# Optimization experiments

Hardware: AMD Instinct MI355X
Metric: run time of the kernel (lower is better)

Reference implementation:

```python
import jax, jax.numpy as jnp
import numpy as np

B, S, H, L, C = 32, 512, 768, 512, 3  # batch, seq, hidden, max_length, num_classes


def _lin_init(k, fan_in, shape):
    return jax.random.normal(k, shape, jnp.float32) * (1.0 / np.sqrt(fan_in))


def setup_inputs() -> dict:
    key = jax.random.key(0)
    ks = jax.random.split(key, 18)
    return {
        "tokens": jax.random.normal(ks[0], (B, S, H), jnp.float32),
        # shared Q/K/V projections (used for both token- and feature-attention)
        "Wq": _lin_init(ks[1], H, (H, H)), "bq": jnp.zeros((H,), jnp.float32),
        "Wk": _lin_init(ks[2], H, (H, H)), "bk": jnp.zeros((H,), jnp.float32),
        "Wv": _lin_init(ks[3], H, (H, H)), "bv": jnp.zeros((H,), jnp.float32),
        # TSGSA: Linear(H,1)+ReLU gate over tokens
        "W_ts": _lin_init(ks[4], H, (H, 1)), "b_ts": jnp.zeros((1,), jnp.float32),
        # FSGSA: Linear(max_length,1)+ReLU gate over padded seq axis (also reused for FGSA per source bug)
        "W_fs": _lin_init(ks[5], L, (L, 1)), "b_fs": jnp.zeros((1,), jnp.float32),
        # TGSA: Linear(H,H)+Sigmoid gate
        "W_tg": _lin_init(ks[6], H, (H, H)), "b_tg": jnp.zeros((H,), jnp.float32),
        # fnn: Linear(7H,H) -> Linear(H,C)
        "W1": _lin_init(ks[7], 7 * H, (7 * H, H)), "b1": jnp.zeros((H,), jnp.float32),
        "W2": _lin_init(ks[8], H, (H, C)), "b2": jnp.zeros((C,), jnp.float32),
    }


def _ln(x):
    # LayerNorm over (seq, hidden) jointly, eps=1e-8; freshly-instantiated affine params are identity
    m = jnp.mean(x, axis=(1, 2), keepdims=True)
    v = jnp.var(x, axis=(1, 2), keepdims=True)
    return (x - m) * jax.lax.rsqrt(v + 1e-8)


def reference(tokens, Wq, bq, Wk, bk, Wv, bv, W_ts, b_ts, W_fs, b_fs, W_tg, b_tg, W1, b1, W2, b2):
    scale = 1.0 / np.sqrt(H)
    Q = tokens @ Wq + bq  # [B,S,H]
    K = tokens @ Wk + bk
    V = tokens @ Wv + bv
    # token-direction self-attention: softmax(Q K^T / sqrt(H)) V
    att = jax.nn.softmax(jnp.einsum('bsh,bth->bst', Q, K) * scale, axis=-1)  # [B,S,S]
    TSA = jnp.einsum('bst,bth->bsh', att, V)
    # feature-direction self-attention: V @ softmax(Q^T K / sqrt(H))
    attN = jax.nn.softmax(jnp.einsum('bsh,bsg->bhg', Q, K) * scale, axis=-1)  # [B,H,H]
    FSA = jnp.einsum('bsh,bhg->bsg', V, attN)
    # gate branches
    TSGSA = jax.nn.relu(tokens @ W_ts + b_ts) * tokens  # [B,S,1]*[B,S,H]
    tpad = jnp.pad(tokens.transpose(0, 2, 1), ((0, 0), (0, 0), (0, L - S)))  # [B,H,L]
    gate_f = jax.nn.relu(tpad @ W_fs + b_fs)  # [B,H,1]
    FSGSA = (gate_f * tokens.transpose(0, 2, 1)).transpose(0, 2, 1)  # [B,S,H]
    TGSA = jax.nn.sigmoid(tokens @ W_tg + b_tg) * tokens
    FGSA = FSGSA  # source bug: FGSA branch applies self.FSGSA, identical to FSGSA
    out_all = jnp.concatenate(
        [tokens, _ln(TSA), _ln(FSA), _ln(TGSA), _ln(FGSA), _ln(TSGSA), _ln(FSGSA)], axis=2)  # [B,S,7H]
    pooled = jnp.mean(out_all, axis=1)  # [B,7H]
    return (pooled @ W1 + b1) @ W2 + b2  # [B,C]
```

## Files before the change

kernel.cpp:

```cpp
#include <hip/hip_runtime.h>
#include <cmath>

typedef unsigned short u16;
typedef __attribute__((ext_vector_type(4))) float f32x4;
typedef __attribute__((ext_vector_type(4))) unsigned int u32x4;
typedef __attribute__((ext_vector_type(8))) __bf16 bf16x8;

__device__ __forceinline__ u16 f2b(float f) {
  unsigned int u = __builtin_bit_cast(unsigned int, f);
  return (u16)((u + 0x7fffu + ((u >> 16) & 1u)) >> 16);
}
__device__ __forceinline__ float b2f(u16 h) {
  unsigned int u = ((unsigned int)h) << 16;
  return __builtin_bit_cast(float, u);
}

__device__ __forceinline__ void glds16(const u16* g, u16* l) {
  __builtin_amdgcn_global_load_lds(
      (const __attribute__((address_space(1))) void*)g,
      (__attribute__((address_space(3))) void*)l, 16, 0, 0);
}

template <int EPI>
__global__ __launch_bounds__(256) void gemm_f_k(
    const u16* __restrict__ Ap, const u16* __restrict__ Bp, u16* __restrict__ Cp,
    u16* __restrict__ CpT, const float* __restrict__ bias,
    const u16* __restrict__ tokp, float* __restrict__ colsum,
    float* __restrict__ bstat, int K, int lda, int ldb, int ldc, long sA,
    long sB, long sC, float scale) {
  __shared__ alignas(16) u16 smem[4][4096];
  __shared__ float scol_s[128];
  __shared__ float sred[2];

  const int gx = gridDim.x, gxy = gx * gridDim.y;
  const int nwg = gxy * gridDim.z;
  int orig = (blockIdx.z * gridDim.y + blockIdx.y) * gx + blockIdx.x;
  int gwi = (orig & 7) * (nwg >> 3) + (orig >> 3);
  const int z = gwi / gxy;
  int rem = gwi - z * gxy;
  const int ty = rem / gx, tx = rem - ty * gx;
  const int tileM = ty << 7, tileN = tx << 7;

  const u16* Abase = Ap + (size_t)z * sA;
  const u16* Bbase = Bp + (size_t)z * sB;

  const int tid = threadIdx.x;
  const int lane = tid & 63, w = tid >> 6;
  const int wr = (w >> 1) << 6, wc = (w & 1) << 6;
  const int fr = lane & 15, fg = lane >> 4;

  f32x4 acc[4][4];
#pragma unroll
  for (int i = 0; i < 4; ++i)
#pragma unroll
    for (int j = 0; j < 4; ++j) acc[i][j] = (f32x4){0.f, 0.f, 0.f, 0.f};

  const int srow = (w << 5) + (lane >> 2);
  const int scol = (((lane & 3) ^ ((lane >> 3) & 3)) << 3);
  const u16* gA = Abase + (size_t)(tileM + srow) * lda + scol;
  const u16* gB = Bbase + (size_t)(tileN + srow) * ldb + scol;
  const int ldsw = (w << 5) * 32;

  auto STAGE = [&](int buf, int k0) {
    const u16* ga = gA + k0;
    const u16* gb = gB + k0;
    u16* la = &smem[buf * 2][ldsw];
    u16* lb = &smem[buf * 2 + 1][ldsw];
    glds16(ga, la);
    glds16(ga + (size_t)16 * lda, la + 512);
    glds16(gb, lb);
    glds16(gb + (size_t)16 * ldb, lb + 512);
  };

  const int col_off = ((fg ^ ((fr >> 1) & 3)) << 3);

  const int nt = K >> 5;
  STAGE(0, 0);
  int cur = 0;
  for (int t = 0; t < nt; ++t) {
    if (t + 1 < nt) {
      STAGE(cur ^ 1, (t + 1) << 5);
      asm volatile("s_waitcnt vmcnt(4)" ::: "memory");
    } else {
      asm volatile("s_waitcnt vmcnt(0)" ::: "memory");
    }
    __builtin_amdgcn_s_barrier();
    asm volatile("" ::: "memory");
    const u16* Ab = smem[cur * 2];
    const u16* Bb = smem[cur * 2 + 1];
    bf16x8 av[4], bw[4];
#pragma unroll
    for (int m = 0; m < 4; ++m)
      av[m] = *(const bf16x8*)&Ab[(wr + (m << 4) + fr) * 32 + col_off];
#pragma unroll
    for (int n = 0; n < 4; ++n)
      bw[n] = *(const bf16x8*)&Bb[(wc + (n << 4) + fr) * 32 + col_off];
#pragma unroll
    for (int m = 0; m < 4; ++m)
#pragma unroll
      for (int n = 0; n < 4; ++n)
        acc[m][n] =
            __builtin_amdgcn_mfma_f32_16x16x32_bf16(av[m], bw[n], acc[m][n], 0, 0, 0);
    asm volatile("" ::: "memory");
    __builtin_amdgcn_s_barrier();
    cur ^= 1;
  }

  if constexpr (EPI == 0) {
    const int cbuf = tileN / 768;
    const int nbase = tileN - cbuf * 768;
    u16* Cz = Cp + (size_t)cbuf * sC;
#pragma unroll
    for (int m = 0; m < 4; ++m) {
#pragma unroll
      for (int n = 0; n < 4; ++n) {
        const int gcol = tileN + wc + (n << 4) + fr;
        const int lcol = nbase + wc + (n << 4) + fr;
        const float bv2 = bias[gcol];
#pragma unroll
        for (int r = 0; r < 4; ++r) {
          const int grow = tileM + wr + (m << 4) + (fg << 2) + r;
          Cz[(size_t)grow * 768 + lcol] = f2b(acc[m][n][r] + bv2);
        }
      }
    }
    u16* tr = &smem[0][0];
    const int xr = fr << 3;
#pragma unroll
    for (int m = 0; m < 4; ++m) {
#pragma unroll
      for (int n = 0; n < 4; ++n) {
        const int gcol = tileN + wc + (n << 4) + fr;
        const float bv2 = bias[gcol];
        union { u16 u[4]; unsigned long long q; } pk;
#pragma unroll
        for (int r = 0; r < 4; ++r) pk.u[r] = f2b(acc[m][n][r] + bv2);
        const int rowb = wr + (m << 4) + (fg << 2);
        *(unsigned long long*)&tr[(wc + (n << 4) + fr) * 128 + (rowb ^ xr)] = pk.q;
      }
    }
    __syncthreads();
    u16* Ct = CpT + (size_t)cbuf * sC;
    const int col = tid >> 1, rh = (tid & 1) << 6;
    const int xc = (col & 15) << 3;
    const u16* trc = &tr[col * 128];
    u16* outc = &Ct[(size_t)(nbase + col) * 16384 + tileM];
#pragma unroll
    for (int i = 0; i < 8; ++i) {
      const int r0 = rh + (i << 3);
      *(u32x4*)&outc[r0] = *(const u32x4*)&trc[r0 ^ xc];
    }
  } else if constexpr (EPI == 1) {
    if (tid < 128) scol_s[tid] = 0.f;
    if (tid == 0) { sred[0] = 0.f; sred[1] = 0.f; }
    __syncthreads();
    float ls = 0.f, lq = 0.f;
#pragma unroll
    for (int n = 0; n < 4; ++n) {
      float cpart = 0.f;
      const int gcol = tileN + wc + (n << 4) + fr;
      const float bv2 = bias[gcol];
#pragma unroll
      for (int m = 0; m < 4; ++m) {
#pragma unroll
        for (int r = 0; r < 4; ++r) {
          const int grow = tileM + wr + (m << 4) + (fg << 2) + r;
          float g = 1.f / (1.f + __expf(-(acc[m][n][r] + bv2)));
          float v = g * b2f(tokp[(size_t)grow * 768 + gcol]);
          cpart += v; ls += v; lq += v * v;
        }
      }
      atomicAdd(&scol_s[wc + (n << 4) + fr], cpart);
    }
    atomicAdd(&sred[0], ls);
    atomicAdd(&sred[1], lq);
    __syncthreads();
    const int b = tileM >> 9;
    if (tid < 128) atomicAdd(&colsum[(size_t)b * 768 + tileN + tid], scol_s[tid]);
    if (tid == 0) {
      atomicAdd(&bstat[b], sred[0]);
      atomicAdd(&bstat[32 + b], sred[1]);
    }
  } else if constexpr (EPI == 2) {
    u16* Cz = Cp + (size_t)z * sC;
#pragma unroll
    for (int m = 0; m < 4; ++m) {
#pragma unroll
      for (int n = 0; n < 4; ++n) {
        const int gcol = tileN + wc + (n << 4) + fr;
#pragma unroll
        for (int r = 0; r < 4; ++r) {
          const int grow = tileM + wr + (m << 4) + (fg << 2) + r;
          Cz[(size_t)grow * ldc + gcol] = f2b(acc[m][n][r] * scale);
        }
      }
    }
  } else {
    if (tid < 128) scol_s[tid] = 0.f;
    if (tid == 0) { sred[0] = 0.f; sred[1] = 0.f; }
    __syncthreads();
    float ls = 0.f, lq = 0.f;
#pragma unroll
    for (int n = 0; n < 4; ++n) {
      float cpart = 0.f;
#pragma unroll
      for (int m = 0; m < 4; ++m) {
#pragma unroll
        for (int r = 0; r < 4; ++r) {
          float v = acc[m][n][r];
          cpart += v; ls += v; lq += v * v;
        }
      }
      atomicAdd(&scol_s[wc + (n << 4) + fr], cpart);
    }
    atomicAdd(&sred[0], ls);
    atomicAdd(&sred[1], lq);
    __syncthreads();
    if (tid < 128) atomicAdd(&colsum[(size_t)z * 768 + tileN + tid], scol_s[tid]);
    if (tid == 0) {
      atomicAdd(&bstat[z], sred[0]);
      atomicAdd(&bstat[32 + z], sred[1]);
    }
  }
}

__global__ __launch_bounds__(256) void cvt_row_k(
    const float* __restrict__ tok, u16* __restrict__ tokb,
    const float* __restrict__ Wts, const float* __restrict__ bts,
    float* __restrict__ gate_t, float* __restrict__ rowsum,
    float* __restrict__ rowsumsq) {
  const int w = threadIdx.x >> 6, lane = threadIdx.x & 63;
  const int row = blockIdx.x * 4 + w;
  const float* p = tok + (size_t)row * 768;
  u16* q = tokb + (size_t)row * 768;
  float s = 0.f, sq = 0.f, g = 0.f;
#pragma unroll
  for (int i = 0; i < 3; ++i) {
    const int idx = (i * 64 + lane) << 2;
    f32x4 v = *(const f32x4*)(p + idx);
    f32x4 wv = *(const f32x4*)(Wts + idx);
    union { u16 u[4]; unsigned long long q8; } pk;
#pragma unroll
    for (int j = 0; j < 4; ++j) {
      s += v[j]; sq += v[j] * v[j]; g += v[j] * wv[j];
      pk.u[j] = f2b(v[j]);
    }
    *(unsigned long long*)(q + idx) = pk.q8;
  }
#pragma unroll
  for (int o = 32; o > 0; o >>= 1) {
    s += __shfl_xor(s, o); sq += __shfl_xor(sq, o); g += __shfl_xor(g, o);
  }
  if (lane == 0) {
    gate_t[row] = fmaxf(g + bts[0], 0.f);
    rowsum[row] = s;
    rowsumsq[row] = sq;
  }
}

__global__ __launch_bounds__(256) void transpose_w_k(const float* __restrict__ W,
                                                     u16* __restrict__ WT) {
  __shared__ float t[64][65];
  const int r0 = blockIdx.y << 6, c0 = blockIdx.x << 6;
  for (int i = threadIdx.x; i < 4096; i += 256) {
    int r = i >> 6, c = i & 63;
    t[r][c] = W[(size_t)(r0 + r) * 768 + c0 + c];
  }
  __syncthreads();
  for (int i = threadIdx.x; i < 4096; i += 256) {
    int rr = i >> 6, cc = i & 63;
    WT[(size_t)(c0 + rr) * 768 + r0 + cc] = f2b(t[cc][rr]);
  }
}

template <int LEN>
__global__ __launch_bounds__(256) void softmax_k(u16* __restrict__ data) {
  constexpr int NP = LEN / 256;
  const int row = blockIdx.x, tid = threadIdx.x;
  u16* p = data + (size_t)row * LEN;
  const int lane = tid & 63, wid = tid >> 6;
  float v[NP];
  float mx = -1e30f;
#pragma unroll
  for (int i = 0; i < NP; ++i) { v[i] = b2f(p[tid + (i << 8)]); mx = fmaxf(mx, v[i]); }
#pragma unroll
  for (int o = 32; o > 0; o >>= 1) mx = fmaxf(mx, __shfl_xor(mx, o));
  __shared__ float red[4], red2[4];
  if (lane == 0) red[wid] = mx;
  __syncthreads();
  mx = fmaxf(fmaxf(red[0], red[1]), fmaxf(red[2], red[3]));
  float sum = 0.f;
#pragma unroll
  for (int i = 0; i < NP; ++i) { v[i] = __expf(v[i] - mx); sum += v[i]; }
#pragma unroll
  for (int o = 32; o > 0; o >>= 1) sum += __shfl_xor(sum, o);
  if (lane == 0) red2[wid] = sum;
  __syncthreads();
  sum = red2[0] + red2[1] + red2[2] + red2[3];
  const float inv = 1.f / sum;
#pragma unroll
  for (int i = 0; i < NP; ++i) p[tid + (i << 8)] = f2b(v[i] * inv);
}

__global__ __launch_bounds__(256) void colsoftmax_k(u16* __restrict__ data) {
  const int b = blockIdx.x;
  const int l = threadIdx.x & 63, st = threadIdx.x >> 6;
  const int h = (blockIdx.y << 6) + l;
  u16* p = data + (size_t)b * 589824 + h;
  const int g0 = st * 192;
  float m = -1e30f, s = 0.f;
#pragma unroll 4
  for (int g = g0; g < g0 + 192; ++g) {
    float v = b2f(p[(size_t)g * 768]);
    float mn = fmaxf(m, v);
    s = s * __expf(m - mn) + __expf(v - mn);
    m = mn;
  }
  __shared__ float sm[4][64], ss[4][64];
  sm[st][l] = m; ss[st][l] = s;
  __syncthreads();
  const float M = fmaxf(fmaxf(sm[0][l], sm[1][l]), fmaxf(sm[2][l], sm[3][l]));
  const float S = ss[0][l] * __expf(sm[0][l] - M) + ss[1][l] * __expf(sm[1][l] - M) +
                  ss[2][l] * __expf(sm[2][l] - M) + ss[3][l] * __expf(sm[3][l] - M);
  const float inv = 1.f / S;
#pragma unroll 4
  for (int g = g0; g < g0 + 192; ++g) {
    float v = b2f(p[(size_t)g * 768]);
    p[(size_t)g * 768] = f2b(__expf(v - M) * inv);
  }
}

__global__ __launch_bounds__(256) void col_stats_k(
    const u16* __restrict__ tokb, const float* __restrict__ Wfs,
    const float* __restrict__ bfs, const float* __restrict__ gate_t,
    float* __restrict__ gate_f, float* __restrict__ colsum_tok,
    float* __restrict__ colsumsq_tok, float* __restrict__ colsum_tsg) {
  const int b = blockIdx.x, h = blockIdx.y * 256 + threadIdx.x;
  const u16* p = tokb + (size_t)b * 512 * 768 + h;
  const float* gt = gate_t + b * 512;
  float cs = 0.f, cq = 0.f, gf = 0.f, tg = 0.f;
#pragma unroll 4
  for (int s = 0; s < 512; ++s) {
    float t = b2f(p[(size_t)s * 768]);
    cs += t; cq += t * t; gf += t * Wfs[s]; tg += t * gt[s];
  }
  const int idx = b * 768 + h;
  gate_f[idx] = fmaxf(gf + bfs[0], 0.f);
  colsum_tok[idx] = cs;
  colsumsq_tok[idx] = cq;
  colsum_tsg[idx] = tg;
}

__global__ __launch_bounds__(256) void batch_stats_k(
    const float* __restrict__ gate_t, const float* __restrict__ rowsum,
    const float* __restrict__ rowsumsq, const float* __restrict__ gate_f,
    const float* __restrict__ colsum_tok, const float* __restrict__ colsumsq_tok,
    float* __restrict__ st) {
  __shared__ float red[4][256];
  const int b = blockIdx.x, tid = threadIdx.x;
  float ts = 0.f, tq = 0.f, fs = 0.f, fq = 0.f;
  for (int s = tid; s < 512; s += 256) {
    float g = gate_t[b * 512 + s];
    ts += g * rowsum[b * 512 + s];
    tq += g * g * rowsumsq[b * 512 + s];
  }
  for (int h = tid; h < 768; h += 256) {
    float g = gate_f[b * 768 + h];
    fs += g * colsum_tok[b * 768 + h];
    fq += g * g * colsumsq_tok[b * 768 + h];
  }
  red[0][tid] = ts; red[1][tid] = tq; red[2][tid] = fs; red[3][tid] = fq;
  __syncthreads();
  for (int o = 128; o > 0; o >>= 1) {
    if (tid < o) {
      red[0][tid] += red[0][tid + o];
      red[1][tid] += red[1][tid + o];
      red[2][tid] += red[2][tid + o];
      red[3][tid] += red[3][tid + o];
    }
    __syncthreads();
  }
  if (tid == 0) {
    st[b] = red[0][0]; st[32 + b] = red[1][0];
    st[64 + b] = red[2][0]; st[96 + b] = red[3][0];
  }
}

__global__ __launch_bounds__(768) void pooled_k(
    const float* __restrict__ colsum_tok, const float* __restrict__ colsum_tsa,
    const float* __restrict__ bstat_tsa, const float* __restrict__ colsum_fsa,
    const float* __restrict__ bstat_fsa, const float* __restrict__ colsum_tgsa,
    const float* __restrict__ bstat_tgsa, const float* __restrict__ colsum_tsg,
    const float* __restrict__ gate_f, const float* __restrict__ st,
    float* __restrict__ pooled) {
  const int b = blockIdx.x, h = threadIdx.x;
  const float invS = 1.f / 512.f, invN = 1.f / (512.f * 768.f);
  const int i = b * 768 + h;
  float* pr = pooled + (size_t)b * 5376;
  pr[h] = colsum_tok[i] * invS;
  auto lnslot = [&](int slot, float cs, float bs, float bq) {
    float m = bs * invN;
    float var = bq * invN - m * m;
    pr[slot * 768 + h] = (cs * invS - m) * rsqrtf(var + 1e-8f);
  };
  lnslot(1, colsum_tsa[i], bstat_tsa[b], bstat_tsa[32 + b]);
  lnslot(2, colsum_fsa[i], bstat_fsa[b], bstat_fsa[32 + b]);
  lnslot(3, colsum_tgsa[i], bstat_tgsa[b], bstat_tgsa[32 + b]);
  const float fsg_cs = gate_f[i] * colsum_tok[i];
  lnslot(4, fsg_cs, st[64 + b], st[96 + b]);
  lnslot(5, colsum_tsg[i], st[b], st[32 + b]);
  lnslot(6, fsg_cs, st[64 + b], st[96 + b]);
}

__global__ __launch_bounds__(256) void fnn1_k(const float* __restrict__ pooled,
                                              const float* __restrict__ W1,
                                              float* __restrict__ tmp1) {
  __shared__ float sp[128][36];
  const int c0 = blockIdx.x << 7, k0 = blockIdx.y << 7;
  const int tid = threadIdx.x;
  for (int i = tid; i < 4096; i += 256) {
    int b = i >> 7, j = i & 127;
    sp[j][b] = pooled[(size_t)b * 5376 + k0 + j];
  }
  __syncthreads();
  const int c = c0 + (tid & 127);
  const int u = (tid >> 7) << 4;
  float acc[16];
#pragma unroll
  for (int t = 0; t < 16; ++t) acc[t] = 0.f;
#pragma unroll 4
  for (int j = 0; j < 128; ++j) {
    float w = W1[(size_t)(k0 + j) * 768 + c];
    const f32x4* row = (const f32x4*)&sp[j][u];
#pragma unroll
    for (int t4 = 0; t4 < 4; ++t4) {
      f32x4 v = row[t4];
#pragma unroll
      for (int r = 0; r < 4; ++r) acc[t4 * 4 + r] += v[r] * w;
    }
  }
#pragma unroll
  for (int t = 0; t < 16; ++t) atomicAdd(&tmp1[(u + t) * 768 + c], acc[t]);
}

__global__ __launch_bounds__(256) void fnn2_k(const float* __restrict__ tmp1,
                                              const float* __restrict__ b1,
                                              const float* __restrict__ W2,
                                              const float* __restrict__ b2,
                                              float* __restrict__ out) {
  const int gw = blockIdx.x * 4 + (threadIdx.x >> 6);
  const int lane = threadIdx.x & 63;
  const int b = gw / 3, c = gw % 3;
  float a = 0.f;
#pragma unroll
  for (int i = 0; i < 12; ++i) {
    int k = lane + i * 64;
    a += (tmp1[b * 768 + k] + b1[k]) * W2[k * 3 + c];
  }
#pragma unroll
  for (int o = 32; o > 0; o >>= 1) a += __shfl_xor(a, o);
  if (lane == 0) out[b * 3 + c] = a + b2[c];
}

extern "C" void kernel_launch(void* const* d_in, const int* in_sizes, int n_in,
                              void* d_out, int out_size, void* d_ws, size_t ws_size,
                              hipStream_t stream) {
  const float* tokens = (const float*)d_in[0];
  const float* Wq = (const float*)d_in[1];
  const float* bq = (const float*)d_in[2];
  const float* Wk = (const float*)d_in[3];
  const float* bk = (const float*)d_in[4];
  const float* Wv = (const float*)d_in[5];
  const float* bv = (const float*)d_in[6];
  const float* Wts = (const float*)d_in[7];
  const float* bts = (const float*)d_in[8];
  const float* Wfs = (const float*)d_in[9];
  const float* bfs = (const float*)d_in[10];
  const float* Wtg = (const float*)d_in[11];
  const float* btg = (const float*)d_in[12];
  const float* W1 = (const float*)d_in[13];
  const float* b1 = (const float*)d_in[14];
  const float* W2 = (const float*)d_in[15];
  const float* b2 = (const float*)d_in[16];
  float* out = (float*)d_out;

  char* ws = (char*)d_ws;
  size_t off = 0;
  auto take = [&](size_t bytes) -> char* {
    char* p = ws + off;
    off += (bytes + 255) & ~(size_t)255;
    return p;
  };
  u16* tokb = (u16*)take((size_t)16384 * 768 * 2);
  u16* WqT = (u16*)take((size_t)768 * 768 * 2);
  u16* WkT = (u16*)take((size_t)768 * 768 * 2);
  u16* WvT = (u16*)take((size_t)768 * 768 * 2);
  u16* WtgT = (u16*)take((size_t)768 * 768 * 2);
  u16* Qb = (u16*)take((size_t)16384 * 768 * 2);
  u16* Kb = (u16*)take((size_t)16384 * 768 * 2);
  u16* Vb = (u16*)take((size_t)16384 * 768 * 2);
  u16* Qt = (u16*)take((size_t)768 * 16384 * 2);
  u16* Kt = (u16*)take((size_t)768 * 16384 * 2);
  u16* Vt = (u16*)take((size_t)768 * 16384 * 2);
  u16* attb = (u16*)take((size_t)32 * 512 * 512 * 2);
  u16* attNt = (u16*)take((size_t)32 * 768 * 768 * 2);
  float* bias3 = (float*)take(2304 * 4);
  char* zbase = ws + off;
  float* colsum_tsa = (float*)take(24576 * 4);
  float* colsum_fsa = (float*)take(24576 * 4);
  float* colsum_tgsa = (float*)take(24576 * 4);
  float* bstat_tsa = (float*)take(64 * 4);
  float* bstat_fsa = (float*)take(64 * 4);
  float* bstat_tgsa = (float*)take(64 * 4);
  float* tmp1 = (float*)take((size_t)32 * 768 * 4);
  size_t zbytes = (size_t)((ws + off) - zbase);
  float* colsum_tsg = (float*)take(24576 * 4);
  float* gate_t = (float*)take(16384 * 4);
  float* rowsum = (float*)take(16384 * 4);
  float* rowsumsq = (float*)take(16384 * 4);
  float* gate_f = (float*)take(24576 * 4);
  float* colsum_tok = (float*)take(24576 * 4);
  float* colsumsq_tok = (float*)take(24576 * 4);
  float* st4 = (float*)take(128 * 4);
  float* pooled = (float*)take((size_t)32 * 5376 * 4);

  hipMemsetAsync(zbase, 0, zbytes, stream);
  hipMemcpyAsync(bias3, bq, 768 * 4, hipMemcpyDeviceToDevice, stream);
  hipMemcpyAsync(bias3 + 768, bk, 768 * 4, hipMemcpyDeviceToDevice, stream);
  hipMemcpyAsync(bias3 + 1536, bv, 768 * 4, hipMemcpyDeviceToDevice, stream);

  const float scale = 1.0f / sqrtf(768.0f);
  const dim3 blk(256);

  cvt_row_k<<<4096, blk, 0, stream>>>(tokens, tokb, Wts, bts, gate_t, rowsum,
                                      rowsumsq);
  transpose_w_k<<<dim3(12, 12), blk, 0, stream>>>(Wq, WqT);
  transpose_w_k<<<dim3(12, 12), blk, 0, stream>>>(Wk, WkT);
  transpose_w_k<<<dim3(12, 12), blk, 0, stream>>>(Wv, WvT);
  transpose_w_k<<<dim3(12, 12), blk, 0, stream>>>(Wtg, WtgT);

  gemm_f_k<0><<<dim3(18, 128, 1), blk, 0, stream>>>(
      tokb, WqT, Qb, Qt, bias3, nullptr, nullptr, nullptr, 768, 768, 768, 768,
      0, 0, 12582912, 0.f);
  gemm_f_k<1><<<dim3(6, 128, 1), blk, 0, stream>>>(
      tokb, WtgT, nullptr, nullptr, btg, tokb, colsum_tgsa, bstat_tgsa, 768,
      768, 768, 0, 0, 0, 0, 0.f);

  gemm_f_k<2><<<dim3(6, 6, 32), blk, 0, stream>>>(
      Kt, Qt, attNt, nullptr, nullptr, nullptr, nullptr, nullptr, 512, 16384,
      16384, 768, 512, 512, 589824, scale);
  colsoftmax_k<<<dim3(32, 12), blk, 0, stream>>>(attNt);

  gemm_f_k<2><<<dim3(4, 4, 32), blk, 0, stream>>>(
      Qb, Kb, attb, nullptr, nullptr, nullptr, nullptr, nullptr, 768, 768, 768,
      512, 393216, 393216, 262144, scale);
  softmax_k<512><<<16384, 256, 0, stream>>>(attb);

  gemm_f_k<3><<<dim3(6, 4, 32), blk, 0, stream>>>(
      attb, Vt, nullptr, nullptr, nullptr, nullptr, colsum_tsa, bstat_tsa, 512,
      512, 16384, 0, 262144, 512, 0, 0.f);
  gemm_f_k<3><<<dim3(6, 4, 32), blk, 0, stream>>>(
      Vb, attNt, nullptr, nullptr, nullptr, nullptr, colsum_fsa, bstat_fsa, 768,
      768, 768, 0, 393216, 589824, 0, 0.f);

  col_stats_k<<<dim3(32, 3), blk, 0, stream>>>(tokb, Wfs, bfs, gate_t, gate_f,
                                               colsum_tok, colsumsq_tok, colsum_tsg);
  batch_stats_k<<<32, blk, 0, stream>>>(gate_t, rowsum, rowsumsq, gate_f,
                                        colsum_tok, colsumsq_tok, st4);

  pooled_k<<<32, 768, 0, stream>>>(colsum_tok, colsum_tsa, bstat_tsa, colsum_fsa,
                                   bstat_fsa, colsum_tgsa, bstat_tgsa, colsum_tsg,
                                   gate_f, st4, pooled);
  fnn1_k<<<dim3(6, 42), blk, 0, stream>>>(pooled, W1, tmp1);
  fnn2_k<<<24, blk, 0, stream>>>(tmp1, b1, W2, b2, out);
}
```

Measured before the change: 479.2 us.

## Stage column softmax through LDS tiles and write transposed GEMM output directly

The column softmax kernel now loads 32x64 tiles with 16-byte vector loads into shared memory and runs the online max/sum per column from LDS. The normalization pass works the same way and writes tiles back vectorized, replacing strided 2-byte global accesses. In the QKV GEMM epilogue, the LDS transpose staging and its barrier are removed, and the transposed output is written directly as 8-byte packed stores. This gives up the fully coalesced 16-byte transposed stores in exchange for less LDS traffic and synchronization. The softmax kernel adds several barriers per chunk.

```diff
diff --git a/kernel.cpp b/kernel.cpp
--- a/kernel.cpp
+++ b/kernel.cpp
@@ -124,31 +124,19 @@
         }
       }
     }
-    u16* tr = &smem[0][0];
-    const int xr = fr << 3;
+    u16* Ct = CpT + (size_t)cbuf * sC;
 #pragma unroll
     for (int m = 0; m < 4; ++m) {
 #pragma unroll
       for (int n = 0; n < 4; ++n) {
         const int gcol = tileN + wc + (n << 4) + fr;
-        const float bv2 = bias[gcol];
+        const int lcol = nbase + wc + (n << 4) + fr;
+        const int grow0 = tileM + wr + (m << 4) + (fg << 2);
         union { u16 u[4]; unsigned long long q; } pk;
 #pragma unroll
-        for (int r = 0; r < 4; ++r) pk.u[r] = f2b(acc[m][n][r] + bv2);
-        const int rowb = wr + (m << 4) + (fg << 2);
-        *(unsigned long long*)&tr[(wc + (n << 4) + fr) * 128 + (rowb ^ xr)] = pk.q;
+        for (int r = 0; r < 4; ++r) pk.u[r] = f2b(acc[m][n][r] + bias[gcol]);
+        *(unsigned long long*)&Ct[(size_t)lcol * 16384 + grow0] = pk.q;
       }
-    }
-    __syncthreads();
-    u16* Ct = CpT + (size_t)cbuf * sC;
-    const int col = tid >> 1, rh = (tid & 1) << 6;
-    const int xc = (col & 15) << 3;
-    const u16* trc = &tr[col * 128];
-    u16* outc = &Ct[(size_t)(nbase + col) * 16384 + tileM];
-#pragma unroll
-    for (int i = 0; i < 8; ++i) {
-      const int r0 = rh + (i << 3);
-      *(u32x4*)&outc[r0] = *(const u32x4*)&trc[r0 ^ xc];
     }
   } else if constexpr (EPI == 1) {
     if (tid < 128) scol_s[tid] = 0.f;
@@ -303,30 +291,45 @@
 }
 
 __global__ __launch_bounds__(256) void colsoftmax_k(u16* __restrict__ data) {
+  __shared__ u16 tile[32][72];
+  __shared__ float sm[4][64], ss[4][64];
+  const int tid = threadIdx.x;
   const int b = blockIdx.x;
-  const int l = threadIdx.x & 63, st = threadIdx.x >> 6;
-  const int h = (blockIdx.y << 6) + l;
-  u16* p = data + (size_t)b * 589824 + h;
-  const int g0 = st * 192;
+  u16* base = data + (size_t)b * 589824 + (blockIdx.y << 6);
+  const int lr = tid >> 3, seg = (tid & 7) << 3;
+  const int c = tid & 63, q = tid >> 6;
   float m = -1e30f, s = 0.f;
-#pragma unroll 4
-  for (int g = g0; g < g0 + 192; ++g) {
-    float v = b2f(p[(size_t)g * 768]);
-    float mn = fmaxf(m, v);
-    s = s * __expf(m - mn) + __expf(v - mn);
-    m = mn;
-  }
-  __shared__ float sm[4][64], ss[4][64];
-  sm[st][l] = m; ss[st][l] = s;
+  for (int ch = 0; ch < 24; ++ch) {
+    u16* g = base + (size_t)(ch * 32 + lr) * 768 + seg;
+    *(u32x4*)&tile[lr][seg] = *(const u32x4*)g;
+    __syncthreads();
+#pragma unroll
+    for (int i = 0; i < 8; ++i) {
+      float v = b2f(tile[(q << 3) + i][c]);
+      float mn = fmaxf(m, v);
+      s = s * __expf(m - mn) + __expf(v - mn);
+      m = mn;
+    }
+    __syncthreads();
+  }
+  sm[q][c] = m; ss[q][c] = s;
   __syncthreads();
-  const float M = fmaxf(fmaxf(sm[0][l], sm[1][l]), fmaxf(sm[2][l], sm[3][l]));
-  const float S = ss[0][l] * __expf(sm[0][l] - M) + ss[1][l] * __expf(sm[1][l] - M) +
-                  ss[2][l] * __expf(sm[2][l] - M) + ss[3][l] * __expf(sm[3][l] - M);
+  const float M = fmaxf(fmaxf(sm[0][c], sm[1][c]), fmaxf(sm[2][c], sm[3][c]));
+  const float S = ss[0][c] * __expf(sm[0][c] - M) + ss[1][c] * __expf(sm[1][c] - M) +
+                  ss[2][c] * __expf(sm[2][c] - M) + ss[3][c] * __expf(sm[3][c] - M);
   const float inv = 1.f / S;
-#pragma unroll 4
-  for (int g = g0; g < g0 + 192; ++g) {
-    float v = b2f(p[(size_t)g * 768]);
-    p[(size_t)g * 768] = f2b(__expf(v - M) * inv);
+  for (int ch = 0; ch < 24; ++ch) {
+    u16* g = base + (size_t)(ch * 32 + lr) * 768 + seg;
+    *(u32x4*)&tile[lr][seg] = *(const u32x4*)g;
+    __syncthreads();
+#pragma unroll
+    for (int i = 0; i < 8; ++i) {
+      const int r = (q << 3) + i;
+      tile[r][c] = f2b(__expf(b2f(tile[r][c]) - M) * inv);
+    }
+    __syncthreads();
+    *(u32x4*)g = *(const u32x4*)&tile[lr][seg];
+    __syncthreads();
   }
 }
 
```

Result: faster. 450.5 us (-6.0%).
